# Kernel optimization log

Measured on AMD Instinct MI355X. Metric: run time of the kernel, lower is better.

## Reference

```python
import jax, jax.numpy as jnp
import numpy as np
import math

B, C_IN, C_OUT, W, H = 16, 64, 64, 256, 128
KW = 7  # conv kernel (1, 7), valid padding -> H' = H - 6


def _conv(x, w, b):
    # NCHW input, OIHW weight, valid padding, stride 1 (matches nn.Conv2d)
    y = jax.lax.conv_general_dilated(x, w, (1, 1), 'VALID',
                                     dimension_numbers=('NCHW', 'OIHW', 'NCHW'))
    return y + b[None, :, None, None]


def setup_inputs() -> dict:
    key = jax.random.key(0)
    ks = jax.random.split(key, 7)
    scale = 1.0 / math.sqrt(C_IN * KW)
    x = jax.random.normal(ks[0], (B, C_IN, W, H), jnp.float32)
    wK = jax.random.normal(ks[1], (C_OUT, C_IN, 1, KW), jnp.float32) * scale
    bK = jax.random.normal(ks[2], (C_OUT,), jnp.float32) * scale
    wQ = jax.random.normal(ks[3], (C_OUT, C_IN, 1, KW), jnp.float32) * scale
    bQ = jax.random.normal(ks[4], (C_OUT,), jnp.float32) * scale
    wV = jax.random.normal(ks[5], (C_OUT, C_IN, 1, KW), jnp.float32) * scale
    bV = jax.random.normal(ks[6], (C_OUT,), jnp.float32) * scale
    return {'x': x, 'wK': wK, 'bK': bK, 'wQ': wQ, 'bQ': bQ, 'wV': wV, 'bV': bV}


def reference(x, wK, bK, wQ, bQ, wV, bV):
    b, c, w, h = x.shape
    # raw row-major flatten of NCHW conv output into (B, W, C*H') -- faithful
    # to torch's .reshape(nbatches, w, -1) on a contiguous tensor
    k = _conv(x, wK, bK).reshape(b, w, -1)   # [B, W, C_OUT*(H-6)]
    q = _conv(x, wQ, bQ).reshape(b, w, -1)   # [B, W, C_OUT*(H-6)]
    v = x.reshape(b, w, -1)                  # [B, W, C_IN*H]
    d_k = q.shape[-1]
    scores = jnp.einsum('bqd,bkd->bqk', q, k) / math.sqrt(d_k)  # [B, W, W]
    i = jnp.arange(w)[:, None]
    j = jnp.arange(w)[None, :]
    blocked = ((i < 128) & (j < 128)) | ((i >= 128) & (j >= 128))
    scores = jnp.where(blocked, -jnp.inf, scores)
    p = jax.nn.softmax(scores, axis=-1)
    x1 = jnp.einsum('bqk,bkd->bqd', p, v).reshape(b, c, w, h)
    y = _conv(x1 + x, wV, bV)                # [B, C_OUT, W, H-6]
    return jnp.where(y >= 0, y, 0.2 * y)     # LeakyReLU(0.2)
```

## Files before the change

### kernel.cpp

```cpp
#include <hip/hip_runtime.h>
#include <hip/hip_bf16.h>

using uint32 = unsigned int;
using u16 = unsigned short;
using short8 = __attribute__((ext_vector_type(8))) short;
using f32x4  = __attribute__((ext_vector_type(4))) float;

__device__ __forceinline__ float bf2f(u16 u) {
  union { uint32 i; float f; } c; c.i = ((uint32)u) << 16; return c.f;
}
__device__ __forceinline__ u16 f2bf(float f) {
  union { float f; uint32 i; } c; c.f = f;
  uint32 u = c.i;
  u += 0x7fffu + ((u >> 16) & 1u);
  return (u16)(u >> 16);
}
__device__ __forceinline__ uint32 pack2(float a, float b) {
  return (uint32)f2bf(a) | ((uint32)f2bf(b) << 16);
}


__global__ __launch_bounds__(256) void prep_weights(
    const float* __restrict__ wK, const float* __restrict__ wQ,
    const float* __restrict__ wV,
    u16* __restrict__ pK, u16* __restrict__ pQ, u16* __restrict__ pV)
{
  int idx = blockIdx.x * 256 + threadIdx.x;
  if (idx >= 86016) return;
  int set = idx / 28672;
  int r = idx - set * 28672;
  int kw = r >> 12;
  int rem = r & 4095;
  int co = rem >> 6, ci = rem & 63;
  const float* src = set == 0 ? wK : (set == 1 ? wQ : wV);
  u16* dst = set == 0 ? pK : (set == 1 ? pQ : pV);
  dst[r] = f2bf(src[co * 448 + ci * 7 + kw]);
}

__global__ __launch_bounds__(256) void conv_kq_mfma(
    const float* __restrict__ x,
    const u16* __restrict__ wpK, const u16* __restrict__ wpQ,
    const float* __restrict__ bK, const float* __restrict__ bQ,
    u16* __restrict__ qbuf, u16* __restrict__ kbuf)
{
  __shared__ u16 xt[136 * 64];
  const int bid = blockIdx.x;
  const int b = bid >> 8, w = bid & 255;
  const int t = threadIdx.x;
  const int lane = t & 63, wv = t >> 6;
  const int ln = lane & 15, g = lane >> 4;

  {
    const float* xb = x + (size_t)b * 2097152 + (size_t)w * 128;
    #pragma unroll
    for (int it = 0; it < 8; ++it) {
      int idx = t + it * 256;
      int h = idx & 127, gq = idx >> 7;
      int ci0 = gq * 4;
      float v0 = xb[(size_t)(ci0 + 0) * 32768 + h];
      float v1 = xb[(size_t)(ci0 + 1) * 32768 + h];
      float v2 = xb[(size_t)(ci0 + 2) * 32768 + h];
      float v3 = xb[(size_t)(ci0 + 3) * 32768 + h];
      uint2 pk;
      pk.x = pack2(v0, v1);
      pk.y = pack2(v2, v3);
      int col = ci0 ^ ((h & 7) << 3);
      *reinterpret_cast<uint2*>(&xt[h * 64 + col]) = pk;
    }
    if (t < 128) {
      int h = 128 + (t >> 4), gq = t & 15;
      *reinterpret_cast<uint2*>(&xt[h * 64 + gq * 4]) = make_uint2(0u, 0u);
    }
  }
  __syncthreads();

  f32x4 accK[8], accQ[8];
  #pragma unroll
  for (int j = 0; j < 8; ++j) { accK[j] = (f32x4)0.f; accQ[j] = (f32x4)0.f; }

  for (int kw = 0; kw < 7; ++kw) {
    #pragma unroll
    for (int ks = 0; ks < 2; ++ks) {
      const int kb = ks * 32 + g * 8;
      const size_t woff = (size_t)(kw * 64 + wv * 16 + ln) * 64 + kb;
      short8 aK = *reinterpret_cast<const short8*>(wpK + woff);
      short8 aQ = *reinterpret_cast<const short8*>(wpQ + woff);
      #pragma unroll
      for (int j = 0; j < 8; ++j) {
        int row = j * 16 + ln + kw;
        int col = kb ^ ((row & 7) << 3);
        short8 bf = *reinterpret_cast<const short8*>(&xt[row * 64 + col]);
        accK[j] = __builtin_amdgcn_mfma_f32_16x16x32_bf16(aK, bf, accK[j], 0, 0, 0);
        accQ[j] = __builtin_amdgcn_mfma_f32_16x16x32_bf16(aQ, bf, accQ[j], 0, 0, 0);
      }
    }
  }

  #pragma unroll
  for (int r = 0; r < 4; ++r) {
    int co = wv * 16 + g * 4 + r;
    float bk = bK[co], bq = bQ[co];
    size_t base = ((size_t)(b * 64 + co) * 256 + w) * 122;
    #pragma unroll
    for (int j = 0; j < 8; ++j) {
      int n = j * 16 + ln;
      if (n < 122) {
        kbuf[base + n] = f2bf(accK[j][r] + bk);
        qbuf[base + n] = f2bf(accQ[j][r] + bq);
      }
    }
  }
}

__global__ __launch_bounds__(256) void scores_mfma(
    const u16* __restrict__ qbuf, const u16* __restrict__ kbuf,
    float* __restrict__ pbuf)
{
  __shared__ float lmax[4][16];
  __shared__ float lsum[4][16];
  const int bid = blockIdx.x;
  const int b = bid & 15, rt = bid >> 4;
  const int t = threadIdx.x;
  const int lane = t & 63, wq = t >> 6;
  const int g = lane >> 4, ln = lane & 15;
  const int i0 = rt * 16;
  const int jbase = (rt < 8) ? 128 : 0;

  const u16* qp  = qbuf + (size_t)(b * 256 + i0 + ln) * 7808 + g * 8;
  const u16* kp0 = kbuf + (size_t)(b * 256 + jbase + wq * 32 + ln) * 7808 + g * 8;
  const u16* kp1 = kp0 + (size_t)16 * 7808;

  f32x4 acc0 = (f32x4)0.f, acc1 = (f32x4)0.f;
  #pragma unroll 4
  for (int c = 0; c < 244; ++c) {
    short8 af = *reinterpret_cast<const short8*>(qp + c * 32);
    short8 b0 = *reinterpret_cast<const short8*>(kp0 + c * 32);
    short8 b1 = *reinterpret_cast<const short8*>(kp1 + c * 32);
    acc0 = __builtin_amdgcn_mfma_f32_16x16x32_bf16(af, b0, acc0, 0, 0, 0);
    acc1 = __builtin_amdgcn_mfma_f32_16x16x32_bf16(af, b1, acc1, 0, 0, 0);
  }

  const float scale = 0.011316967f;
  float s0[4], s1[4];
  #pragma unroll
  for (int r = 0; r < 4; ++r) { s0[r] = acc0[r] * scale; s1[r] = acc1[r] * scale; }

  float pm[4], ps[4];
  #pragma unroll
  for (int r = 0; r < 4; ++r) {
    float m = fmaxf(s0[r], s1[r]);
    #pragma unroll
    for (int off = 8; off >= 1; off >>= 1) m = fmaxf(m, __shfl_xor(m, off));
    float e = __expf(s0[r] - m) + __expf(s1[r] - m);
    #pragma unroll
    for (int off = 8; off >= 1; off >>= 1) e += __shfl_xor(e, off);
    pm[r] = m; ps[r] = e;
  }
  if (ln == 0) {
    #pragma unroll
    for (int r = 0; r < 4; ++r) {
      lmax[wq][g * 4 + r] = pm[r];
      lsum[wq][g * 4 + r] = ps[r];
    }
  }
  __syncthreads();

  #pragma unroll
  for (int r = 0; r < 4; ++r) {
    int row = g * 4 + r;
    float m0 = lmax[0][row], m1 = lmax[1][row], m2 = lmax[2][row], m3 = lmax[3][row];
    float mm = fmaxf(fmaxf(m0, m1), fmaxf(m2, m3));
    float ss = lsum[0][row] * __expf(m0 - mm) + lsum[1][row] * __expf(m1 - mm)
             + lsum[2][row] * __expf(m2 - mm) + lsum[3][row] * __expf(m3 - mm);
    float inv = 1.0f / ss;
    float p0 = __expf(s0[r] - mm) * inv;
    float p1 = __expf(s1[r] - mm) * inv;
    float* prow = pbuf + (size_t)(b * 256 + i0 + row) * 128 + wq * 32 + ln;
    prow[0]  = p0;
    prow[16] = p1;
  }
}

__global__ __launch_bounds__(256) void pv_mfma(
    const float* __restrict__ pbuf, const float* __restrict__ x,
    u16* __restrict__ zbuf)
{
  __shared__ u16 pl[128 * 136];
  __shared__ u16 vt[256 * 40];
  const int bid = blockIdx.x;
  const int b  = bid >> 6;
  const int hb = (bid >> 5) & 1;
  const int ec = bid & 31;
  const int t = threadIdx.x;
  const int lane = t & 63, wv = t >> 6;
  const int ln = lane & 15, g = lane >> 4;

  const int i0 = hb ? 0 : 128;
  const int jbase = hb ? 128 : 0;
  const int e0 = ec * 256;
  const float* xb = x + (size_t)b * 2097152;
  const float* pb = pbuf + (size_t)(b * 256 + i0) * 128;

  uint32* plw = reinterpret_cast<uint32*>(pl);
  #pragma unroll
  for (int it = 0; it < 32; ++it) {
    int idx = t + it * 256;
    int ii = idx >> 6, jjp = idx & 63;
    float2 f2 = *reinterpret_cast<const float2*>(pb + ii * 128 + jjp * 2);
    plw[ii * 68 + jjp] = pack2(f2.x, f2.y);
  }

  f32x4 acc[2][16];
  #pragma unroll
  for (int mt = 0; mt < 2; ++mt)
    #pragma unroll
    for (int nt = 0; nt < 16; ++nt) acc[mt][nt] = (f32x4)0.f;

  uint32* vtw = reinterpret_cast<uint32*>(vt);
  for (int ks = 0; ks < 4; ++ks) {
    __syncthreads();
    #pragma unroll
    for (int it = 0; it < 16; ++it) {
      int idx = t + it * 256;
      int e = idx & 255, jp = idx >> 8;
      const float* vr = xb + (size_t)(jbase + ks * 32 + jp * 2) * 8192 + e0 + e;
      float f0 = vr[0];
      float f1 = vr[8192];
      vtw[e * 20 + jp] = pack2(f0, f1);
    }
    __syncthreads();
    short8 af[2];
    #pragma unroll
    for (int mt = 0; mt < 2; ++mt) {
      int row = wv * 32 + mt * 16 + ln;
      af[mt] = *reinterpret_cast<const short8*>(&pl[row * 136 + ks * 32 + g * 8]);
    }
    #pragma unroll
    for (int nt = 0; nt < 16; ++nt) {
      int e = nt * 16 + ln;
      short8 bf = *reinterpret_cast<const short8*>(&vt[e * 40 + g * 8]);
      acc[0][nt] = __builtin_amdgcn_mfma_f32_16x16x32_bf16(af[0], bf, acc[0][nt], 0, 0, 0);
      acc[1][nt] = __builtin_amdgcn_mfma_f32_16x16x32_bf16(af[1], bf, acc[1][nt], 0, 0, 0);
    }
  }

  #pragma unroll
  for (int mt = 0; mt < 2; ++mt) {
    #pragma unroll
    for (int r = 0; r < 4; ++r) {
      int i = i0 + wv * 32 + mt * 16 + g * 4 + r;
      const float* xr = xb + (size_t)i * 8192 + e0 + ln;
      u16* zr = zbuf + (size_t)(b * 256 + i) * 8192 + e0 + ln;
      #pragma unroll
      for (int nt = 0; nt < 16; ++nt) {
        float z = xr[nt * 16] + acc[mt][nt][r];
        zr[nt * 16] = f2bf(z);
      }
    }
  }
}

__global__ __launch_bounds__(256) void conv_out_mfma(
    const u16* __restrict__ zbuf, const u16* __restrict__ wpV,
    const float* __restrict__ bV, float* __restrict__ out)
{
  __shared__ u16 xt[136 * 64];
  const int bid = blockIdx.x;
  const int b = bid >> 8, w = bid & 255;
  const int t = threadIdx.x;
  const int lane = t & 63, wv = t >> 6;
  const int ln = lane & 15, g = lane >> 4;

  {
    const u16* zb = zbuf + (size_t)b * 2097152 + (size_t)w * 128;
    #pragma unroll
    for (int it = 0; it < 8; ++it) {
      int idx = t + it * 256;
      int h = idx & 127, gq = idx >> 7;
      int ci0 = gq * 4;
      u16 v0 = zb[(size_t)(ci0 + 0) * 32768 + h];
      u16 v1 = zb[(size_t)(ci0 + 1) * 32768 + h];
      u16 v2 = zb[(size_t)(ci0 + 2) * 32768 + h];
      u16 v3 = zb[(size_t)(ci0 + 3) * 32768 + h];
      uint2 pk;
      pk.x = (uint32)v0 | ((uint32)v1 << 16);
      pk.y = (uint32)v2 | ((uint32)v3 << 16);
      int col = ci0 ^ ((h & 7) << 3);
      *reinterpret_cast<uint2*>(&xt[h * 64 + col]) = pk;
    }
    if (t < 128) {
      int h = 128 + (t >> 4), gq = t & 15;
      *reinterpret_cast<uint2*>(&xt[h * 64 + gq * 4]) = make_uint2(0u, 0u);
    }
  }
  __syncthreads();

  f32x4 acc[8];
  #pragma unroll
  for (int j = 0; j < 8; ++j) acc[j] = (f32x4)0.f;

  for (int kw = 0; kw < 7; ++kw) {
    #pragma unroll
    for (int ks = 0; ks < 2; ++ks) {
      const int kb = ks * 32 + g * 8;
      const size_t woff = (size_t)(kw * 64 + wv * 16 + ln) * 64 + kb;
      short8 aV = *reinterpret_cast<const short8*>(wpV + woff);
      #pragma unroll
      for (int j = 0; j < 8; ++j) {
        int row = j * 16 + ln + kw;
        int col = kb ^ ((row & 7) << 3);
        short8 bf = *reinterpret_cast<const short8*>(&xt[row * 64 + col]);
        acc[j] = __builtin_amdgcn_mfma_f32_16x16x32_bf16(aV, bf, acc[j], 0, 0, 0);
      }
    }
  }

  #pragma unroll
  for (int r = 0; r < 4; ++r) {
    int co = wv * 16 + g * 4 + r;
    float bv = bV[co];
    size_t base = ((size_t)(b * 64 + co) * 256 + w) * 122;
    #pragma unroll
    for (int j = 0; j < 8; ++j) {
      int n = j * 16 + ln;
      if (n < 122) {
        float y = acc[j][r] + bv;
        out[base + n] = (y >= 0.f) ? y : 0.2f * y;
      }
    }
  }
}

extern "C" void kernel_launch(void* const* d_in, const int* in_sizes, int n_in,
                              void* d_out, int out_size, void* d_ws, size_t ws_size,
                              hipStream_t stream) {
  const float* x  = (const float*)d_in[0];
  const float* wK = (const float*)d_in[1];
  const float* bK = (const float*)d_in[2];
  const float* wQ = (const float*)d_in[3];
  const float* bQ = (const float*)d_in[4];
  const float* wV = (const float*)d_in[5];
  const float* bV = (const float*)d_in[6];
  float* out = (float*)d_out;

  char* ws = (char*)d_ws;
  u16* qbuf  = (u16*)ws;
  u16* zbuf  = (u16*)ws;
  u16* kbuf  = (u16*)(ws + 67108864);
  float* pbuf = (float*)(ws + 131072000);
  u16* wpK = (u16*)(ws + 133169152);
  u16* wpQ = (u16*)(ws + 133226496);
  u16* wpV = (u16*)(ws + 133283840);

  prep_weights<<<dim3(336), dim3(256), 0, stream>>>(wK, wQ, wV, wpK, wpQ, wpV);
  conv_kq_mfma<<<dim3(16 * 256), dim3(256), 0, stream>>>(x, wpK, wpQ, bK, bQ, qbuf, kbuf);
  scores_mfma<<<dim3(256), dim3(256), 0, stream>>>(qbuf, kbuf, pbuf);
  pv_mfma<<<dim3(1024), dim3(256), 0, stream>>>(pbuf, x, zbuf);
  conv_out_mfma<<<dim3(16 * 256), dim3(256), 0, stream>>>(zbuf, wpV, bV, out);
}
```

Before: 342.6 us.

## Pre-transpose conv inputs to bf16 tiles and load via global_load_lds

Adds prep_x and prep_z kernels that transpose and convert the conv inputs into swizzled bf16 tiles once. The two conv kernels then fill LDS with direct 16-byte global-to-LDS loads instead of strided scalar gathers, and get occupancy hints in their launch bounds. The softmax probabilities are now stored as bf16, which halves pbuf traffic and simplifies the pv load. This adds two extra kernel launches and a full extra write and read of the activations, and the workspace layout is reshuffled with aliasing between buffers.

Result: slower. 395.1 us (+15.3%).

```diff
diff --git a/kernel.cpp b/kernel.cpp
--- a/kernel.cpp
+++ b/kernel.cpp
@@ -17,6 +17,12 @@
 }
 __device__ __forceinline__ uint32 pack2(float a, float b) {
   return (uint32)f2bf(a) | ((uint32)f2bf(b) << 16);
+}
+
+__device__ __forceinline__ void gload_lds16(const void* g, void* l) {
+  __builtin_amdgcn_global_load_lds(
+      (const __attribute__((address_space(1))) unsigned int*)g,
+      (__attribute__((address_space(3))) unsigned int*)l, 16, 0, 0);
 }
 
 
@@ -37,8 +43,66 @@
   dst[r] = f2bf(src[co * 448 + ci * 7 + kw]);
 }
 
-__global__ __launch_bounds__(256) void conv_kq_mfma(
-    const float* __restrict__ x,
+__global__ __launch_bounds__(256) void prep_x(
+    const float* __restrict__ x, u16* __restrict__ xbuf)
+{
+  __shared__ u16 xt[128 * 64];
+  const int bid = blockIdx.x;
+  const int b = bid >> 8, w = bid & 255;
+  const int t = threadIdx.x;
+  const float* xb = x + (size_t)b * 2097152 + (size_t)w * 128;
+  #pragma unroll
+  for (int it = 0; it < 8; ++it) {
+    int idx = t + it * 256;
+    int h = idx & 127, gq = idx >> 7;
+    int ci0 = gq * 4;
+    float v0 = xb[(size_t)(ci0 + 0) * 32768 + h];
+    float v1 = xb[(size_t)(ci0 + 1) * 32768 + h];
+    float v2 = xb[(size_t)(ci0 + 2) * 32768 + h];
+    float v3 = xb[(size_t)(ci0 + 3) * 32768 + h];
+    uint2 pk; pk.x = pack2(v0, v1); pk.y = pack2(v2, v3);
+    int col = ci0 ^ ((h & 7) << 3);
+    *reinterpret_cast<uint2*>(&xt[h * 64 + col]) = pk;
+  }
+  __syncthreads();
+  const uint4* s = reinterpret_cast<const uint4*>(xt);
+  uint4* d = reinterpret_cast<uint4*>(xbuf + (size_t)bid * 8192);
+  #pragma unroll
+  for (int it = 0; it < 4; ++it) d[t + it * 256] = s[t + it * 256];
+}
+
+__global__ __launch_bounds__(256) void prep_z(
+    const u16* __restrict__ zraw, u16* __restrict__ ztbuf)
+{
+  __shared__ u16 xt[128 * 64];
+  const int bid = blockIdx.x;
+  const int b = bid >> 8, w = bid & 255;
+  const int t = threadIdx.x;
+  const u16* zb = zraw + (size_t)b * 2097152 + (size_t)w * 128;
+  #pragma unroll
+  for (int it = 0; it < 8; ++it) {
+    int idx = t + it * 256;
+    int h = idx & 127, gq = idx >> 7;
+    int ci0 = gq * 4;
+    u16 v0 = zb[(size_t)(ci0 + 0) * 32768 + h];
+    u16 v1 = zb[(size_t)(ci0 + 1) * 32768 + h];
+    u16 v2 = zb[(size_t)(ci0 + 2) * 32768 + h];
+    u16 v3 = zb[(size_t)(ci0 + 3) * 32768 + h];
+    uint2 pk;
+    pk.x = (uint32)v0 | ((uint32)v1 << 16);
+    pk.y = (uint32)v2 | ((uint32)v3 << 16);
+    int col = ci0 ^ ((h & 7) << 3);
+    *reinterpret_cast<uint2*>(&xt[h * 64 + col]) = pk;
+  }
+  __syncthreads();
+  const uint4* s = reinterpret_cast<const uint4*>(xt);
+  uint4* d = reinterpret_cast<uint4*>(ztbuf + (size_t)bid * 8192);
+  #pragma unroll
+  for (int it = 0; it < 4; ++it) d[t + it * 256] = s[t + it * 256];
+}
+
+__global__ __launch_bounds__(256, 4) void conv_kq_mfma(
+    const u16* __restrict__ xbuf,
     const u16* __restrict__ wpK, const u16* __restrict__ wpQ,
     const float* __restrict__ bK, const float* __restrict__ bQ,
     u16* __restrict__ qbuf, u16* __restrict__ kbuf)
@@ -51,27 +115,17 @@
   const int ln = lane & 15, g = lane >> 4;
 
   {
-    const float* xb = x + (size_t)b * 2097152 + (size_t)w * 128;
-    #pragma unroll
-    for (int it = 0; it < 8; ++it) {
-      int idx = t + it * 256;
-      int h = idx & 127, gq = idx >> 7;
-      int ci0 = gq * 4;
-      float v0 = xb[(size_t)(ci0 + 0) * 32768 + h];
-      float v1 = xb[(size_t)(ci0 + 1) * 32768 + h];
-      float v2 = xb[(size_t)(ci0 + 2) * 32768 + h];
-      float v3 = xb[(size_t)(ci0 + 3) * 32768 + h];
-      uint2 pk;
-      pk.x = pack2(v0, v1);
-      pk.y = pack2(v2, v3);
-      int col = ci0 ^ ((h & 7) << 3);
-      *reinterpret_cast<uint2*>(&xt[h * 64 + col]) = pk;
+    const u16* src = xbuf + (size_t)bid * 8192;
+    #pragma unroll
+    for (int c = 0; c < 4; ++c) {
+      int chunk = wv * 4 + c;
+      gload_lds16(src + chunk * 512 + lane * 8, &xt[chunk * 512]);
     }
     if (t < 128) {
-      int h = 128 + (t >> 4), gq = t & 15;
-      *reinterpret_cast<uint2*>(&xt[h * 64 + gq * 4]) = make_uint2(0u, 0u);
-    }
-  }
+      *reinterpret_cast<uint2*>(&xt[128 * 64 + t * 4]) = make_uint2(0u, 0u);
+    }
+  }
+  asm volatile("s_waitcnt vmcnt(0)" ::: "memory");
   __syncthreads();
 
   f32x4 accK[8], accQ[8];
@@ -114,7 +168,7 @@
 
 __global__ __launch_bounds__(256) void scores_mfma(
     const u16* __restrict__ qbuf, const u16* __restrict__ kbuf,
-    float* __restrict__ pbuf)
+    u16* __restrict__ pbuf)
 {
   __shared__ float lmax[4][16];
   __shared__ float lsum[4][16];
@@ -175,15 +229,15 @@
     float inv = 1.0f / ss;
     float p0 = __expf(s0[r] - mm) * inv;
     float p1 = __expf(s1[r] - mm) * inv;
-    float* prow = pbuf + (size_t)(b * 256 + i0 + row) * 128 + wq * 32 + ln;
-    prow[0]  = p0;
-    prow[16] = p1;
+    u16* prow = pbuf + (size_t)(b * 256 + i0 + row) * 128 + wq * 32 + ln;
+    prow[0]  = f2bf(p0);
+    prow[16] = f2bf(p1);
   }
 }
 
 __global__ __launch_bounds__(256) void pv_mfma(
-    const float* __restrict__ pbuf, const float* __restrict__ x,
-    u16* __restrict__ zbuf)
+    const u16* __restrict__ pbuf, const float* __restrict__ x,
+    u16* __restrict__ zraw)
 {
   __shared__ u16 pl[128 * 136];
   __shared__ u16 vt[256 * 40];
@@ -199,15 +253,16 @@
   const int jbase = hb ? 128 : 0;
   const int e0 = ec * 256;
   const float* xb = x + (size_t)b * 2097152;
-  const float* pb = pbuf + (size_t)(b * 256 + i0) * 128;
-
-  uint32* plw = reinterpret_cast<uint32*>(pl);
-  #pragma unroll
-  for (int it = 0; it < 32; ++it) {
-    int idx = t + it * 256;
-    int ii = idx >> 6, jjp = idx & 63;
-    float2 f2 = *reinterpret_cast<const float2*>(pb + ii * 128 + jjp * 2);
-    plw[ii * 68 + jjp] = pack2(f2.x, f2.y);
+
+  {
+    const u16* pb = pbuf + (size_t)(b * 256 + i0) * 128;
+    #pragma unroll
+    for (int it = 0; it < 8; ++it) {
+      int idx = t + it * 256;
+      int row = idx >> 4, c = idx & 15;
+      uint4 v = *reinterpret_cast<const uint4*>(pb + row * 128 + c * 8);
+      *reinterpret_cast<uint4*>(&pl[row * 136 + c * 8]) = v;
+    }
   }
 
   f32x4 acc[2][16];
@@ -250,7 +305,7 @@
     for (int r = 0; r < 4; ++r) {
       int i = i0 + wv * 32 + mt * 16 + g * 4 + r;
       const float* xr = xb + (size_t)i * 8192 + e0 + ln;
-      u16* zr = zbuf + (size_t)(b * 256 + i) * 8192 + e0 + ln;
+      u16* zr = zraw + (size_t)(b * 256 + i) * 8192 + e0 + ln;
       #pragma unroll
       for (int nt = 0; nt < 16; ++nt) {
         float z = xr[nt * 16] + acc[mt][nt][r];
@@ -260,8 +315,8 @@
   }
 }
 
-__global__ __launch_bounds__(256) void conv_out_mfma(
-    const u16* __restrict__ zbuf, const u16* __restrict__ wpV,
+__global__ __launch_bounds__(256, 4) void conv_out_mfma(
+    const u16* __restrict__ ztbuf, const u16* __restrict__ wpV,
     const float* __restrict__ bV, float* __restrict__ out)
 {
   __shared__ u16 xt[136 * 64];
@@ -272,27 +327,17 @@
   const int ln = lane & 15, g = lane >> 4;
 
   {
-    const u16* zb = zbuf + (size_t)b * 2097152 + (size_t)w * 128;
-    #pragma unroll
-    for (int it = 0; it < 8; ++it) {
-      int idx = t + it * 256;
-      int h = idx & 127, gq = idx >> 7;
-      int ci0 = gq * 4;
-      u16 v0 = zb[(size_t)(ci0 + 0) * 32768 + h];
-      u16 v1 = zb[(size_t)(ci0 + 1) * 32768 + h];
-      u16 v2 = zb[(size_t)(ci0 + 2) * 32768 + h];
-      u16 v3 = zb[(size_t)(ci0 + 3) * 32768 + h];
-      uint2 pk;
-      pk.x = (uint32)v0 | ((uint32)v1 << 16);
-      pk.y = (uint32)v2 | ((uint32)v3 << 16);
-      int col = ci0 ^ ((h & 7) << 3);
-      *reinterpret_cast<uint2*>(&xt[h * 64 + col]) = pk;
+    const u16* src = ztbuf + (size_t)bid * 8192;
+    #pragma unroll
+    for (int c = 0; c < 4; ++c) {
+      int chunk = wv * 4 + c;
+      gload_lds16(src + chunk * 512 + lane * 8, &xt[chunk * 512]);
     }
     if (t < 128) {
-      int h = 128 + (t >> 4), gq = t & 15;
-      *reinterpret_cast<uint2*>(&xt[h * 64 + gq * 4]) = make_uint2(0u, 0u);
-    }
-  }
+      *reinterpret_cast<uint2*>(&xt[128 * 64 + t * 4]) = make_uint2(0u, 0u);
+    }
+  }
+  asm volatile("s_waitcnt vmcnt(0)" ::: "memory");
   __syncthreads();
 
   f32x4 acc[8];
@@ -345,16 +390,20 @@
 
   char* ws = (char*)d_ws;
   u16* qbuf  = (u16*)ws;
-  u16* zbuf  = (u16*)ws;
-  u16* kbuf  = (u16*)(ws + 67108864);
-  float* pbuf = (float*)(ws + 131072000);
-  u16* wpK = (u16*)(ws + 133169152);
-  u16* wpQ = (u16*)(ws + 133226496);
-  u16* wpV = (u16*)(ws + 133283840);
+  u16* pbuf  = (u16*)(ws + 63963136);
+  u16* wpK   = (u16*)(ws + 65011712);
+  u16* wpQ   = (u16*)(ws + 65069056);
+  u16* kbuf  = (u16*)(ws + 65126400);
+  u16* xbuf  = (u16*)(ws + 129089536);
+  u16* zraw  = xbuf;
+  u16* wpV   = (u16*)(ws + 196198400);
+  u16* ztbuf = (u16*)ws;
 
   prep_weights<<<dim3(336), dim3(256), 0, stream>>>(wK, wQ, wV, wpK, wpQ, wpV);
-  conv_kq_mfma<<<dim3(16 * 256), dim3(256), 0, stream>>>(x, wpK, wpQ, bK, bQ, qbuf, kbuf);
+  prep_x<<<dim3(16 * 256), dim3(256), 0, stream>>>(x, xbuf);
+  conv_kq_mfma<<<dim3(16 * 256), dim3(256), 0, stream>>>(xbuf, wpK, wpQ, bK, bQ, qbuf, kbuf);
   scores_mfma<<<dim3(256), dim3(256), 0, stream>>>(qbuf, kbuf, pbuf);
-  pv_mfma<<<dim3(1024), dim3(256), 0, stream>>>(pbuf, x, zbuf);
-  conv_out_mfma<<<dim3(16 * 256), dim3(256), 0, stream>>>(zbuf, wpV, bV, out);
-}
+  pv_mfma<<<dim3(1024), dim3(256), 0, stream>>>(pbuf, x, zraw);
+  prep_z<<<dim3(16 * 256), dim3(256), 0, stream>>>(zraw, ztbuf);
+  conv_out_mfma<<<dim3(16 * 256), dim3(256), 0, stream>>>(ztbuf, wpV, bV, out);
+}
```
